# Optimization experiments

Measured on AMD Instinct MI355X. Metric: run time of the kernel, lower is better.

The kernel has to match this reference:

```python
import jax, jax.numpy as jnp
import numpy as np

EMBED_DIM = 1024
N_HEADS = 16
HEAD_DIM = EMBED_DIM // N_HEADS
EPS = 1e-6


def setup_inputs() -> dict:
    key = jax.random.key(0)
    k_x, k_wqkv, k_bqkv, k_wo, k_bo = jax.random.split(key, 5)
    B, T, C = 2, 2048, EMBED_DIM
    s = 1.0 / np.sqrt(C)
    return {
        "x": jax.random.normal(k_x, (B, T, C), dtype=jnp.float32),
        "w_qkv": jax.random.normal(k_wqkv, (C, 3 * C), dtype=jnp.float32) * s,
        "b_qkv": jax.random.normal(k_bqkv, (3 * C,), dtype=jnp.float32) * s,
        "w_out": jax.random.normal(k_wo, (C, C), dtype=jnp.float32) * s,
        "b_out": jax.random.normal(k_bo, (C,), dtype=jnp.float32) * s,
    }


def reference(x, w_qkv, b_qkv, w_out, b_out):
    B, T, C = x.shape
    H, D = N_HEADS, HEAD_DIM
    qkv = x @ w_qkv + b_qkv                       # [B,T,3C]
    q, k, v = jnp.split(qkv, 3, axis=-1)
    # [B,H,T,D]
    q = q.reshape(B, T, H, D).transpose(0, 2, 1, 3)
    k = k.reshape(B, T, H, D).transpose(0, 2, 1, 3)
    v = v.reshape(B, T, H, D).transpose(0, 2, 1, 3)
    dot = jnp.einsum("bhqd,bhkd->bhqk", q, k)     # [B,H,T,T]
    q_sq = jnp.sum(q * q, axis=-1)[..., :, None]  # [B,H,T,1]
    k_sq = jnp.sum(k * k, axis=-1)[..., None, :]  # [B,H,1,T]
    scores = (dot * dot) / (q_sq + k_sq - 2.0 * dot + EPS)
    causal = jnp.tril(jnp.ones((T, T), dtype=bool))
    scores = jnp.where(causal, scores, -jnp.inf)
    attn = jax.nn.softmax(scores, axis=-1)
    out = jnp.einsum("bhqk,bhkd->bhqd", attn, v)  # [B,H,T,D]
    out = out.transpose(0, 2, 1, 3).reshape(B, T, C)
    return out @ w_out + b_out
```

## Files before the change

### kernel.cpp

```cpp
#include <hip/hip_runtime.h>
#include <stdint.h>


#define TSEQ 2048
#define BATCH 2

typedef _Float16 f16x8 __attribute__((ext_vector_type(8)));
typedef float f32x4 __attribute__((ext_vector_type(4)));

#define MFMA16(a, b, c) __builtin_amdgcn_mfma_f32_16x16x32_f16(a, b, c, 0, 0, 0)

__device__ __forceinline__ unsigned short f2h(float f) {
  union { _Float16 h; unsigned short u; } v;
  v.h = (_Float16)f;
  return v.u;
}
__device__ __forceinline__ float h2f(unsigned short u) {
  union { unsigned short u; _Float16 h; } v;
  v.u = u;
  return (float)v.h;
}
__device__ __forceinline__ unsigned int pack2h(float lo, float hi) {
  return (unsigned int)f2h(lo) | ((unsigned int)f2h(hi) << 16);
}
__device__ __forceinline__ float sumsq_u32(unsigned int u) {
  float lo = h2f(u & 0xffffu);
  float hi = h2f(u >> 16);
  return lo * lo + hi * hi;
}
__device__ __forceinline__ void async_ld16(const void* g, const void* l) {
  __builtin_amdgcn_global_load_lds((const __attribute__((address_space(1))) void*)g,
                                   (__attribute__((address_space(3))) void*)l,
                                   16, 0, 0);
}

__global__ __launch_bounds__(256) void cvt_x(const float* __restrict__ src,
                                             unsigned short* __restrict__ dst) {
  const int i = (blockIdx.x * 256 + threadIdx.x) * 8;
  const float4 a = *(const float4*)(src + i);
  const float4 b = *(const float4*)(src + i + 4);
  uint4 o;
  o.x = pack2h(a.x, a.y); o.y = pack2h(a.z, a.w);
  o.z = pack2h(b.x, b.y); o.w = pack2h(b.z, b.w);
  *(uint4*)(dst + i) = o;
}

__global__ __launch_bounds__(256) void transpose_w(const float* __restrict__ src,
                                                   unsigned short* __restrict__ dst,
                                                   int K, int N) {
  __shared__ unsigned short tile[32][33];
  const int tx = threadIdx.x, ty = threadIdx.y;
  const int nb = blockIdx.x * 32, kb = blockIdx.y * 32;
#pragma unroll
  for (int i = 0; i < 4; i++)
    tile[ty + 8 * i][tx] = f2h(src[(size_t)(kb + ty + 8 * i) * N + nb + tx]);
  __syncthreads();
#pragma unroll
  for (int i = 0; i < 4; i++)
    dst[(size_t)(nb + ty + 8 * i) * K + kb + tx] = tile[tx][ty + 8 * i];
}

template <bool OUT_F32>
__global__ __launch_bounds__(256) void gemm_bt(const unsigned short* __restrict__ A,
                                               const unsigned short* __restrict__ Bt,
                                               const float* __restrict__ bias,
                                               void* __restrict__ Cp,
                                               int N, int K) {
  __shared__ __attribute__((aligned(16))) unsigned short Atile[128 * 32];
  __shared__ __attribute__((aligned(16))) unsigned short Btile[128 * 32];
  const int tid = threadIdx.x;
  const int w = tid >> 6, lane = tid & 63;
  const int quad = lane >> 4, l15 = lane & 15;
  const int m0 = blockIdx.y * 128, n0 = blockIdx.x * 128;
  const int wr = w >> 1, wc = w & 1;
  f32x4 acc[4][4] = {};
  for (int kt = 0; kt < K; kt += 32) {
    __syncthreads();
#pragma unroll
    for (int it = 0; it < 2; it++) {
      const int c = it * 256 + tid;
      const int row = c >> 2, kc = c & 3;
      async_ld16(A + (size_t)(m0 + row) * K + kt + kc * 8,
                 &Atile[(size_t)(it * 256 + w * 64) * 8]);
      async_ld16(Bt + (size_t)(n0 + row) * K + kt + kc * 8,
                 &Btile[(size_t)(it * 256 + w * 64) * 8]);
    }
    __syncthreads();
    f16x8 af[4], bfr[4];
#pragma unroll
    for (int i = 0; i < 4; i++)
      af[i] = *(const f16x8*)&Atile[(wr * 64 + i * 16 + l15) * 32 + quad * 8];
#pragma unroll
    for (int j = 0; j < 4; j++)
      bfr[j] = *(const f16x8*)&Btile[(wc * 64 + j * 16 + l15) * 32 + quad * 8];
#pragma unroll
    for (int i = 0; i < 4; i++)
#pragma unroll
      for (int j = 0; j < 4; j++)
        acc[i][j] = MFMA16(af[i], bfr[j], acc[i][j]);
  }
#pragma unroll
  for (int j = 0; j < 4; j++) {
    const int n = n0 + wc * 64 + j * 16 + l15;
    const float bv = bias[n];
#pragma unroll
    for (int i = 0; i < 4; i++) {
      const int mb = m0 + wr * 64 + i * 16 + quad * 4;
#pragma unroll
      for (int r = 0; r < 4; r++) {
        if constexpr (OUT_F32)
          ((float*)Cp)[(size_t)(mb + r) * N + n] = acc[i][j][r] + bv;
        else
          ((unsigned short*)Cp)[(size_t)(mb + r) * N + n] = f2h(acc[i][j][r] + bv);
      }
    }
  }
}

__global__ __launch_bounds__(256, 4) void yat_attn(const unsigned short* __restrict__ qkv,
                                                   unsigned short* __restrict__ outp) {
  __shared__ __attribute__((aligned(16))) unsigned short Qp[64 * 72];
  __shared__ __attribute__((aligned(16))) unsigned short Kp[64 * 72];
  __shared__ __attribute__((aligned(16))) unsigned short Vt[64 * 72];
  __shared__ __attribute__((aligned(16))) unsigned short Pl[64 * 72];
  __shared__ float qsq[64], ksq[64], bcast[64];
  const int tid = threadIdx.x;
  const int w = tid >> 6, lane = tid & 63;
  const int quad = lane >> 4, l15 = lane & 15;
  const int bh = blockIdx.x, b = bh >> 4, h = bh & 15;
  const int y = blockIdx.y;
  const int qt = (y < 8) ? 31 - y : (y < 16) ? y - 8 : (y < 24) ? 39 - y : y - 16;
  const unsigned short* base = qkv + (size_t)b * TSEQ * 3072 + h * 64;
  const int t = tid >> 2, dc = (tid & 3) * 16;
  const int d0 = tid & 31, tg8 = tid >> 5;

  {
    const unsigned short* g = base + (size_t)(qt * 64 + t) * 3072 + dc;
    uint4 v0 = *(const uint4*)g;
    uint4 v1 = *(const uint4*)(g + 8);
    *(uint4*)&Qp[t * 72 + dc] = v0;
    *(uint4*)&Qp[t * 72 + dc + 8] = v1;
    float s = sumsq_u32(v0.x) + sumsq_u32(v0.y) + sumsq_u32(v0.z) + sumsq_u32(v0.w) +
              sumsq_u32(v1.x) + sumsq_u32(v1.y) + sumsq_u32(v1.z) + sumsq_u32(v1.w);
    s += __shfl_xor(s, 1);
    s += __shfl_xor(s, 2);
    if ((tid & 3) == 0) qsq[t] = s;
  }

  f32x4 accO[4] = {};
  float m_r[4] = {0.f, 0.f, 0.f, 0.f};
  float l_r[4] = {0.f, 0.f, 0.f, 0.f};

  uint4 kreg0, kreg1;
  unsigned int vreg[8];
  {
    const unsigned short* gk = base + 1024 + (size_t)t * 3072 + dc;
    kreg0 = *(const uint4*)gk;
    kreg1 = *(const uint4*)(gk + 8);
    const unsigned short* gv = base + 2048 + (size_t)(tg8 * 8) * 3072 + 2 * d0;
#pragma unroll
    for (int s = 0; s < 8; s++)
      vreg[s] = *(const unsigned int*)(gv + (size_t)s * 3072);
  }

  for (int kt = 0; kt <= qt; kt++) {
    __syncthreads();
    {
      *(uint4*)&Kp[t * 72 + dc] = kreg0;
      *(uint4*)&Kp[t * 72 + dc + 8] = kreg1;
      float s = sumsq_u32(kreg0.x) + sumsq_u32(kreg0.y) + sumsq_u32(kreg0.z) +
                sumsq_u32(kreg0.w) + sumsq_u32(kreg1.x) + sumsq_u32(kreg1.y) +
                sumsq_u32(kreg1.z) + sumsq_u32(kreg1.w);
      s += __shfl_xor(s, 1);
      s += __shfl_xor(s, 2);
      if ((tid & 3) == 0) ksq[t] = s;
      uint4 LO, HI;
      LO.x = (vreg[0] & 0xffffu) | (vreg[1] << 16);
      LO.y = (vreg[2] & 0xffffu) | (vreg[3] << 16);
      LO.z = (vreg[4] & 0xffffu) | (vreg[5] << 16);
      LO.w = (vreg[6] & 0xffffu) | (vreg[7] << 16);
      HI.x = (vreg[0] >> 16) | (vreg[1] & 0xffff0000u);
      HI.y = (vreg[2] >> 16) | (vreg[3] & 0xffff0000u);
      HI.z = (vreg[4] >> 16) | (vreg[5] & 0xffff0000u);
      HI.w = (vreg[6] >> 16) | (vreg[7] & 0xffff0000u);
      *(uint4*)&Vt[(2 * d0) * 72 + tg8 * 8] = LO;
      *(uint4*)&Vt[(2 * d0 + 1) * 72 + tg8 * 8] = HI;
    }
    if (kt < qt) {
      const unsigned short* gk = base + 1024 + (size_t)((kt + 1) * 64 + t) * 3072 + dc;
      kreg0 = *(const uint4*)gk;
      kreg1 = *(const uint4*)(gk + 8);
      const unsigned short* gv =
          base + 2048 + (size_t)((kt + 1) * 64 + tg8 * 8) * 3072 + 2 * d0;
#pragma unroll
      for (int s = 0; s < 8; s++)
        vreg[s] = *(const unsigned int*)(gv + (size_t)s * 3072);
    }
    __syncthreads();

    f32x4 accS[4] = {};
    const f16x8 aq0 = *(const f16x8*)&Qp[(w * 16 + l15) * 72 + quad * 8];
    const f16x8 aq1 = *(const f16x8*)&Qp[(w * 16 + l15) * 72 + 32 + quad * 8];
#pragma unroll
    for (int nt = 0; nt < 4; nt++) {
      const f16x8 bk0 = *(const f16x8*)&Kp[(nt * 16 + l15) * 72 + quad * 8];
      const f16x8 bk1 = *(const f16x8*)&Kp[(nt * 16 + l15) * 72 + 32 + quad * 8];
      accS[nt] = MFMA16(aq0, bk0, accS[nt]);
      accS[nt] = MFMA16(aq1, bk1, accS[nt]);
    }
    const bool diag = (kt == qt);
    float pval[4][4];
    float tmax[4] = {0.f, 0.f, 0.f, 0.f};
#pragma unroll
    for (int nt = 0; nt < 4; nt++) {
#pragma unroll
      for (int r = 0; r < 4; r++) {
        const int ql = w * 16 + quad * 4 + r;
        const int tl = nt * 16 + l15;
        const float d = accS[nt][r];
        const float den = qsq[ql] + ksq[tl] - 2.f * d + 1e-6f;
        float s = d * d * __builtin_amdgcn_rcpf(den);
        if (diag && tl > ql) s = -1e30f;
        pval[nt][r] = s;
        tmax[r] = fmaxf(tmax[r], s);
      }
    }
#pragma unroll
    for (int r = 0; r < 4; r++) {
      tmax[r] = fmaxf(tmax[r], __shfl_xor(tmax[r], 1));
      tmax[r] = fmaxf(tmax[r], __shfl_xor(tmax[r], 2));
      tmax[r] = fmaxf(tmax[r], __shfl_xor(tmax[r], 4));
      tmax[r] = fmaxf(tmax[r], __shfl_xor(tmax[r], 8));
    }
    float alpha[4];
#pragma unroll
    for (int r = 0; r < 4; r++) {
      const float mn = fmaxf(m_r[r], tmax[r]);
      alpha[r] = __expf(m_r[r] - mn);
      m_r[r] = mn;
    }
#pragma unroll
    for (int nt = 0; nt < 4; nt++)
#pragma unroll
      for (int r = 0; r < 4; r++)
        pval[nt][r] = __expf(pval[nt][r] - m_r[r]);
#pragma unroll
    for (int r = 0; r < 4; r++) {
      float su = pval[0][r] + pval[1][r] + pval[2][r] + pval[3][r];
      su += __shfl_xor(su, 1);
      su += __shfl_xor(su, 2);
      su += __shfl_xor(su, 4);
      su += __shfl_xor(su, 8);
      l_r[r] = l_r[r] * alpha[r] + su;
    }
#pragma unroll
    for (int nt = 0; nt < 4; nt++)
#pragma unroll
      for (int r = 0; r < 4; r++)
        Pl[(w * 16 + quad * 4 + r) * 72 + nt * 16 + l15] = f2h(pval[nt][r]);
    if (l15 == 0) {
#pragma unroll
      for (int r = 0; r < 4; r++) bcast[w * 16 + quad * 4 + r] = alpha[r];
    }
    __syncthreads();

    const float am = bcast[w * 16 + l15];
#pragma unroll
    for (int i = 0; i < 4; i++) {
      accO[i][0] *= am; accO[i][1] *= am; accO[i][2] *= am; accO[i][3] *= am;
    }
    const f16x8 bp0 = *(const f16x8*)&Pl[(w * 16 + l15) * 72 + quad * 8];
    const f16x8 bp1 = *(const f16x8*)&Pl[(w * 16 + l15) * 72 + 32 + quad * 8];
#pragma unroll
    for (int i = 0; i < 4; i++) {
      const f16x8 av0 = *(const f16x8*)&Vt[(i * 16 + l15) * 72 + quad * 8];
      const f16x8 av1 = *(const f16x8*)&Vt[(i * 16 + l15) * 72 + 32 + quad * 8];
      accO[i] = MFMA16(av0, bp0, accO[i]);
      accO[i] = MFMA16(av1, bp1, accO[i]);
    }
  }

  __syncthreads();
  if (l15 == 0) {
#pragma unroll
    for (int r = 0; r < 4; r++) bcast[w * 16 + quad * 4 + r] = l_r[r];
  }
  __syncthreads();
  const float linv = 1.0f / bcast[w * 16 + l15];
#pragma unroll
  for (int i = 0; i < 4; i++)
#pragma unroll
    for (int r = 0; r < 4; r++)
      Qp[(w * 16 + l15) * 72 + i * 16 + quad * 4 + r] = f2h(accO[i][r] * linv);
  __syncthreads();
  {
    uint4 o0 = *(const uint4*)&Qp[t * 72 + dc];
    uint4 o1 = *(const uint4*)&Qp[t * 72 + dc + 8];
    unsigned short* g = outp + (size_t)(b * TSEQ + qt * 64 + t) * 1024 + h * 64 + dc;
    *(uint4*)g = o0;
    *(uint4*)(g + 8) = o1;
  }
}

extern "C" void kernel_launch(void* const* d_in, const int* in_sizes, int n_in,
                              void* d_out, int out_size, void* d_ws, size_t ws_size,
                              hipStream_t stream) {
  (void)in_sizes; (void)n_in; (void)out_size; (void)ws_size;
  const float* x     = (const float*)d_in[0];
  const float* w_qkv = (const float*)d_in[1];
  const float* b_qkv = (const float*)d_in[2];
  const float* w_out = (const float*)d_in[3];
  const float* b_out = (const float*)d_in[4];
  float* out = (float*)d_out;

  unsigned short* wqkvT  = (unsigned short*)d_ws;
  unsigned short* woT    = wqkvT + (size_t)3072 * 1024;
  unsigned short* qkvws  = woT + (size_t)1024 * 1024;
  unsigned short* xh     = qkvws + (size_t)4096 * 3072;
  unsigned short* attnws = xh;

  cvt_x<<<dim3(4096 * 1024 / (256 * 8)), 256, 0, stream>>>(x, xh);
  transpose_w<<<dim3(3072 / 32, 1024 / 32), dim3(32, 8), 0, stream>>>(w_qkv, wqkvT, 1024, 3072);
  transpose_w<<<dim3(1024 / 32, 1024 / 32), dim3(32, 8), 0, stream>>>(w_out, woT, 1024, 1024);
  gemm_bt<false><<<dim3(3072 / 128, 4096 / 128), 256, 0, stream>>>(xh, wqkvT, b_qkv, qkvws, 3072, 1024);
  yat_attn<<<dim3(BATCH * 16, 32), 256, 0, stream>>>(qkvws, attnws);
  gemm_bt<true><<<dim3(1024 / 128, 4096 / 128), 256, 0, stream>>>(attnws, woT, b_out, out, 1024, 1024);
}
```

Before: 226.3 us.

## Enlarge attention query tile to 128 rows and narrow output GEMM N tile

The attention kernel now processes 128 query rows per block with 512 threads (8 waves), so each K/V tile loaded into shared memory is reused by twice as many queries. The Q fragments are hoisted out of the key loop, and the causal mask becomes an offset comparison. The output projection GEMM is templated on N-tile width and launched with 64-wide tiles to double its block count for better occupancy. The risks are lower occupancy from the bigger attention blocks, fewer attention blocks overall, and more wasted masked work on the diagonal tiles.

```diff
diff --git a/kernel.cpp b/kernel.cpp
--- a/kernel.cpp
+++ b/kernel.cpp
@@ -60,48 +60,53 @@
     dst[(size_t)(nb + ty + 8 * i) * K + kb + tx] = tile[tx][ty + 8 * i];
 }
 
-template <bool OUT_F32>
+template <int TN, bool OUT_F32>
 __global__ __launch_bounds__(256) void gemm_bt(const unsigned short* __restrict__ A,
                                                const unsigned short* __restrict__ Bt,
                                                const float* __restrict__ bias,
                                                void* __restrict__ Cp,
                                                int N, int K) {
   __shared__ __attribute__((aligned(16))) unsigned short Atile[128 * 32];
-  __shared__ __attribute__((aligned(16))) unsigned short Btile[128 * 32];
+  __shared__ __attribute__((aligned(16))) unsigned short Btile[TN * 32];
+  constexpr int NJ = TN / 32;
   const int tid = threadIdx.x;
   const int w = tid >> 6, lane = tid & 63;
   const int quad = lane >> 4, l15 = lane & 15;
-  const int m0 = blockIdx.y * 128, n0 = blockIdx.x * 128;
+  const int m0 = blockIdx.y * 128, n0 = blockIdx.x * TN;
   const int wr = w >> 1, wc = w & 1;
-  f32x4 acc[4][4] = {};
+  const int nwc = wc * (TN / 2);
+  f32x4 acc[4][NJ] = {};
   for (int kt = 0; kt < K; kt += 32) {
     __syncthreads();
 #pragma unroll
     for (int it = 0; it < 2; it++) {
       const int c = it * 256 + tid;
-      const int row = c >> 2, kc = c & 3;
-      async_ld16(A + (size_t)(m0 + row) * K + kt + kc * 8,
+      async_ld16(A + (size_t)(m0 + (c >> 2)) * K + kt + (c & 3) * 8,
                  &Atile[(size_t)(it * 256 + w * 64) * 8]);
-      async_ld16(Bt + (size_t)(n0 + row) * K + kt + kc * 8,
+    }
+#pragma unroll
+    for (int it = 0; it < TN / 64; it++) {
+      const int c = it * 256 + tid;
+      async_ld16(Bt + (size_t)(n0 + (c >> 2)) * K + kt + (c & 3) * 8,
                  &Btile[(size_t)(it * 256 + w * 64) * 8]);
     }
     __syncthreads();
-    f16x8 af[4], bfr[4];
+    f16x8 af[4], bfr[NJ];
 #pragma unroll
     for (int i = 0; i < 4; i++)
       af[i] = *(const f16x8*)&Atile[(wr * 64 + i * 16 + l15) * 32 + quad * 8];
 #pragma unroll
-    for (int j = 0; j < 4; j++)
-      bfr[j] = *(const f16x8*)&Btile[(wc * 64 + j * 16 + l15) * 32 + quad * 8];
+    for (int j = 0; j < NJ; j++)
+      bfr[j] = *(const f16x8*)&Btile[(nwc + j * 16 + l15) * 32 + quad * 8];
 #pragma unroll
     for (int i = 0; i < 4; i++)
 #pragma unroll
-      for (int j = 0; j < 4; j++)
+      for (int j = 0; j < NJ; j++)
         acc[i][j] = MFMA16(af[i], bfr[j], acc[i][j]);
   }
 #pragma unroll
-  for (int j = 0; j < 4; j++) {
-    const int n = n0 + wc * 64 + j * 16 + l15;
+  for (int j = 0; j < NJ; j++) {
+    const int n = n0 + nwc + j * 16 + l15;
     const float bv = bias[n];
 #pragma unroll
     for (int i = 0; i < 4; i++) {
@@ -117,90 +122,84 @@
   }
 }
 
-__global__ __launch_bounds__(256, 4) void yat_attn(const unsigned short* __restrict__ qkv,
+__global__ __launch_bounds__(512, 4) void yat_attn(const unsigned short* __restrict__ qkv,
                                                    unsigned short* __restrict__ outp) {
-  __shared__ __attribute__((aligned(16))) unsigned short Qp[64 * 72];
+  __shared__ __attribute__((aligned(16))) unsigned short Qp[128 * 72];
   __shared__ __attribute__((aligned(16))) unsigned short Kp[64 * 72];
   __shared__ __attribute__((aligned(16))) unsigned short Vt[64 * 72];
-  __shared__ __attribute__((aligned(16))) unsigned short Pl[64 * 72];
-  __shared__ float qsq[64], ksq[64], bcast[64];
+  __shared__ __attribute__((aligned(16))) unsigned short Pl[128 * 72];
+  __shared__ float qsq[128], ksq[64], bcast[128];
   const int tid = threadIdx.x;
   const int w = tid >> 6, lane = tid & 63;
   const int quad = lane >> 4, l15 = lane & 15;
   const int bh = blockIdx.x, b = bh >> 4, h = bh & 15;
   const int y = blockIdx.y;
-  const int qt = (y < 8) ? 31 - y : (y < 16) ? y - 8 : (y < 24) ? 39 - y : y - 16;
+  const int yb = (y < 8) ? 15 - y : y - 8;
+  const int ktmax = 2 * yb + 1;
   const unsigned short* base = qkv + (size_t)b * TSEQ * 3072 + h * 64;
-  const int t = tid >> 2, dc = (tid & 3) * 16;
-  const int d0 = tid & 31, tg8 = tid >> 5;
+  const int t2 = tid >> 2, dc = (tid & 3) * 16;
+  const int tk = tid >> 3, dck = (tid & 7) * 8;
+  const int d0 = tid & 31, tg4 = tid >> 5;
 
   {
-    const unsigned short* g = base + (size_t)(qt * 64 + t) * 3072 + dc;
+    const unsigned short* g = base + (size_t)(yb * 128 + t2) * 3072 + dc;
     uint4 v0 = *(const uint4*)g;
     uint4 v1 = *(const uint4*)(g + 8);
-    *(uint4*)&Qp[t * 72 + dc] = v0;
-    *(uint4*)&Qp[t * 72 + dc + 8] = v1;
+    *(uint4*)&Qp[t2 * 72 + dc] = v0;
+    *(uint4*)&Qp[t2 * 72 + dc + 8] = v1;
     float s = sumsq_u32(v0.x) + sumsq_u32(v0.y) + sumsq_u32(v0.z) + sumsq_u32(v0.w) +
               sumsq_u32(v1.x) + sumsq_u32(v1.y) + sumsq_u32(v1.z) + sumsq_u32(v1.w);
     s += __shfl_xor(s, 1);
     s += __shfl_xor(s, 2);
-    if ((tid & 3) == 0) qsq[t] = s;
-  }
+    if ((tid & 3) == 0) qsq[t2] = s;
+  }
+  __syncthreads();
+  const f16x8 aq0 = *(const f16x8*)&Qp[(w * 16 + l15) * 72 + quad * 8];
+  const f16x8 aq1 = *(const f16x8*)&Qp[(w * 16 + l15) * 72 + 32 + quad * 8];
 
   f32x4 accO[4] = {};
   float m_r[4] = {0.f, 0.f, 0.f, 0.f};
   float l_r[4] = {0.f, 0.f, 0.f, 0.f};
 
-  uint4 kreg0, kreg1;
-  unsigned int vreg[8];
+  uint4 kreg;
+  unsigned int vreg[4];
   {
-    const unsigned short* gk = base + 1024 + (size_t)t * 3072 + dc;
-    kreg0 = *(const uint4*)gk;
-    kreg1 = *(const uint4*)(gk + 8);
-    const unsigned short* gv = base + 2048 + (size_t)(tg8 * 8) * 3072 + 2 * d0;
-#pragma unroll
-    for (int s = 0; s < 8; s++)
+    kreg = *(const uint4*)(base + 1024 + (size_t)tk * 3072 + dck);
+    const unsigned short* gv = base + 2048 + (size_t)(tg4 * 4) * 3072 + 2 * d0;
+#pragma unroll
+    for (int s = 0; s < 4; s++)
       vreg[s] = *(const unsigned int*)(gv + (size_t)s * 3072);
   }
 
-  for (int kt = 0; kt <= qt; kt++) {
+  for (int kt = 0; kt <= ktmax; kt++) {
     __syncthreads();
     {
-      *(uint4*)&Kp[t * 72 + dc] = kreg0;
-      *(uint4*)&Kp[t * 72 + dc + 8] = kreg1;
-      float s = sumsq_u32(kreg0.x) + sumsq_u32(kreg0.y) + sumsq_u32(kreg0.z) +
-                sumsq_u32(kreg0.w) + sumsq_u32(kreg1.x) + sumsq_u32(kreg1.y) +
-                sumsq_u32(kreg1.z) + sumsq_u32(kreg1.w);
+      *(uint4*)&Kp[tk * 72 + dck] = kreg;
+      float s = sumsq_u32(kreg.x) + sumsq_u32(kreg.y) + sumsq_u32(kreg.z) +
+                sumsq_u32(kreg.w);
       s += __shfl_xor(s, 1);
       s += __shfl_xor(s, 2);
-      if ((tid & 3) == 0) ksq[t] = s;
-      uint4 LO, HI;
+      s += __shfl_xor(s, 4);
+      if ((tid & 7) == 0) ksq[tk] = s;
+      uint2 LO, HI;
       LO.x = (vreg[0] & 0xffffu) | (vreg[1] << 16);
       LO.y = (vreg[2] & 0xffffu) | (vreg[3] << 16);
-      LO.z = (vreg[4] & 0xffffu) | (vreg[5] << 16);
-      LO.w = (vreg[6] & 0xffffu) | (vreg[7] << 16);
       HI.x = (vreg[0] >> 16) | (vreg[1] & 0xffff0000u);
       HI.y = (vreg[2] >> 16) | (vreg[3] & 0xffff0000u);
-      HI.z = (vreg[4] >> 16) | (vreg[5] & 0xffff0000u);
-      HI.w = (vreg[6] >> 16) | (vreg[7] & 0xffff0000u);
-      *(uint4*)&Vt[(2 * d0) * 72 + tg8 * 8] = LO;
-      *(uint4*)&Vt[(2 * d0 + 1) * 72 + tg8 * 8] = HI;
-    }
-    if (kt < qt) {
-      const unsigned short* gk = base + 1024 + (size_t)((kt + 1) * 64 + t) * 3072 + dc;
-      kreg0 = *(const uint4*)gk;
-      kreg1 = *(const uint4*)(gk + 8);
+      *(uint2*)&Vt[(2 * d0) * 72 + tg4 * 4] = LO;
+      *(uint2*)&Vt[(2 * d0 + 1) * 72 + tg4 * 4] = HI;
+    }
+    if (kt < ktmax) {
+      kreg = *(const uint4*)(base + 1024 + (size_t)((kt + 1) * 64 + tk) * 3072 + dck);
       const unsigned short* gv =
-          base + 2048 + (size_t)((kt + 1) * 64 + tg8 * 8) * 3072 + 2 * d0;
-#pragma unroll
-      for (int s = 0; s < 8; s++)
+          base + 2048 + (size_t)((kt + 1) * 64 + tg4 * 4) * 3072 + 2 * d0;
+#pragma unroll
+      for (int s = 0; s < 4; s++)
         vreg[s] = *(const unsigned int*)(gv + (size_t)s * 3072);
     }
     __syncthreads();
 
     f32x4 accS[4] = {};
-    const f16x8 aq0 = *(const f16x8*)&Qp[(w * 16 + l15) * 72 + quad * 8];
-    const f16x8 aq1 = *(const f16x8*)&Qp[(w * 16 + l15) * 72 + 32 + quad * 8];
 #pragma unroll
     for (int nt = 0; nt < 4; nt++) {
       const f16x8 bk0 = *(const f16x8*)&Kp[(nt * 16 + l15) * 72 + quad * 8];
@@ -208,7 +207,8 @@
       accS[nt] = MFMA16(aq0, bk0, accS[nt]);
       accS[nt] = MFMA16(aq1, bk1, accS[nt]);
     }
-    const bool diag = (kt == qt);
+    const int kdiff = kt * 64 - yb * 128;
+    const bool dz = (kdiff >= 0);
     float pval[4][4];
     float tmax[4] = {0.f, 0.f, 0.f, 0.f};
 #pragma unroll
@@ -220,7 +220,7 @@
         const float d = accS[nt][r];
         const float den = qsq[ql] + ksq[tl] - 2.f * d + 1e-6f;
         float s = d * d * __builtin_amdgcn_rcpf(den);
-        if (diag && tl > ql) s = -1e30f;
+        if (dz && (kdiff + tl > ql)) s = -1e30f;
         pval[nt][r] = s;
         tmax[r] = fmaxf(tmax[r], s);
       }
@@ -294,9 +294,9 @@
       Qp[(w * 16 + l15) * 72 + i * 16 + quad * 4 + r] = f2h(accO[i][r] * linv);
   __syncthreads();
   {
-    uint4 o0 = *(const uint4*)&Qp[t * 72 + dc];
-    uint4 o1 = *(const uint4*)&Qp[t * 72 + dc + 8];
-    unsigned short* g = outp + (size_t)(b * TSEQ + qt * 64 + t) * 1024 + h * 64 + dc;
+    uint4 o0 = *(const uint4*)&Qp[t2 * 72 + dc];
+    uint4 o1 = *(const uint4*)&Qp[t2 * 72 + dc + 8];
+    unsigned short* g = outp + (size_t)(b * TSEQ + yb * 128 + t2) * 1024 + h * 64 + dc;
     *(uint4*)g = o0;
     *(uint4*)(g + 8) = o1;
   }
@@ -322,7 +322,7 @@
   cvt_x<<<dim3(4096 * 1024 / (256 * 8)), 256, 0, stream>>>(x, xh);
   transpose_w<<<dim3(3072 / 32, 1024 / 32), dim3(32, 8), 0, stream>>>(w_qkv, wqkvT, 1024, 3072);
   transpose_w<<<dim3(1024 / 32, 1024 / 32), dim3(32, 8), 0, stream>>>(w_out, woT, 1024, 1024);
-  gemm_bt<false><<<dim3(3072 / 128, 4096 / 128), 256, 0, stream>>>(xh, wqkvT, b_qkv, qkvws, 3072, 1024);
-  yat_attn<<<dim3(BATCH * 16, 32), 256, 0, stream>>>(qkvws, attnws);
-  gemm_bt<true><<<dim3(1024 / 128, 4096 / 128), 256, 0, stream>>>(attnws, woT, b_out, out, 1024, 1024);
-}
+  gemm_bt<128, false><<<dim3(3072 / 128, 4096 / 128), 256, 0, stream>>>(xh, wqkvT, b_qkv, qkvws, 3072, 1024);
+  yat_attn<<<dim3(BATCH * 16, 16), 512, 0, stream>>>(qkvws, attnws);
+  gemm_bt<64, true><<<dim3(1024 / 64, 4096 / 128), 256, 0, stream>>>(attnws, woT, b_out, out, 1024, 1024);
+}
```

Measured after the change: 226.8 us. No clear change (+0.2%).
